# Kernel optimization log

Measured on AMD Instinct MI355X. Metric: run time of the kernel, lower is better.

Reference implementation:

```python
import jax, jax.numpy as jnp
import numpy as np

B, S, D, H = 2, 2048, 1024, 16
E = D // H  # per-head dim_q = dim_k = 64
LN_EPS = 1e-5


def setup_inputs() -> dict:
    key = jax.random.key(0)
    ks = jax.random.split(key, 12)
    s_in = 1.0 / np.sqrt(D)
    s_cat = 1.0 / np.sqrt(H * E)
    return {
        "q": jax.random.normal(ks[0], (B, S, D), jnp.float32),
        "k": jax.random.normal(ks[1], (B, S, D), jnp.float32),
        "v": jax.random.normal(ks[2], (B, S, D), jnp.float32),
        # stacked per-head projection weights [H, D, E] (acts as x @ W + b per head)
        "Wq": jax.random.uniform(ks[3], (H, D, E), jnp.float32, -s_in, s_in),
        "bq": jax.random.uniform(ks[4], (H, E), jnp.float32, -s_in, s_in),
        "Wk": jax.random.uniform(ks[5], (H, D, E), jnp.float32, -s_in, s_in),
        "bk": jax.random.uniform(ks[6], (H, E), jnp.float32, -s_in, s_in),
        "Wv": jax.random.uniform(ks[7], (H, D, E), jnp.float32, -s_in, s_in),
        "bv": jax.random.uniform(ks[8], (H, E), jnp.float32, -s_in, s_in),
        # output linear: [H*E, D]
        "Wo": jax.random.uniform(ks[9], (H * E, D), jnp.float32, -s_cat, s_cat),
        "bo": jax.random.uniform(ks[10], (D,), jnp.float32, -s_cat, s_cat),
        # LayerNorm affine params
        "gamma": jnp.ones((D,), jnp.float32),
        "beta": jnp.zeros((D,), jnp.float32),
    }


def _attention(q, k, v, Wq, bq, Wk, bk, Wv, bv, Wo, bo, gamma, beta):
    # per-head projections: [B,H,S,E]
    qh = jnp.einsum('bsd,hde->bhse', q, Wq) + bq[None, :, None, :]
    kh = jnp.einsum('bsd,hde->bhse', k, Wk) + bk[None, :, None, :]
    vh = jnp.einsum('bsd,hde->bhse', v, Wv) + bv[None, :, None, :]
    scale = jnp.asarray(E, qh.dtype) ** 0.5
    scores = jnp.einsum('bhse,bhte->bhst', qh, kh) / scale  # [B,H,S,S]
    attn = jax.nn.softmax(scores, axis=-1)
    ctx = jnp.einsum('bhst,bhte->bhse', attn, vh)  # [B,H,S,E]
    # concat heads -> [B,S,H*E], then output linear
    cat = ctx.transpose(0, 2, 1, 3).reshape(q.shape[0], q.shape[1], H * E)
    out = cat @ Wo + bo  # [B,S,D]
    # Residual (dropout = identity in eval) + LayerNorm
    x = q + out
    mu = jnp.mean(x, axis=-1, keepdims=True)
    var = jnp.mean((x - mu) ** 2, axis=-1, keepdims=True)
    return (x - mu) * jax.lax.rsqrt(var + LN_EPS) * gamma + beta


def reference(q, k, v, Wq, bq, Wk, bk, Wv, bv, Wo, bo, gamma, beta):
    return _attention(q, k, v, Wq, bq, Wk, bk, Wv, bv, Wo, bo, gamma, beta)
```

## Files before the change

kernel.cpp:

```cpp
#include <hip/hip_runtime.h>
#include <stdint.h>

#define B_  2
#define S_  2048
#define D_  1024
#define H_  16
#define E_  64
#define BH_ 32
#define M_  4096
#define NSPLIT 2
#define KCHUNK (S_ / NSPLIT)

typedef __bf16 bf16x8 __attribute__((ext_vector_type(8)));
typedef float  f32x4  __attribute__((ext_vector_type(4)));
typedef float  f32x16 __attribute__((ext_vector_type(16)));
typedef unsigned short u16;

#define QSCALE 0.180336880f

#define EXP2(x) __builtin_amdgcn_exp2f(x)

__device__ __forceinline__ u16 f2bf(float f) {
  uint32_t u = __builtin_bit_cast(uint32_t, f);
  u = (u + 0x7FFFu + ((u >> 16) & 1u)) >> 16;
  return (u16)u;
}

__device__ __forceinline__ uint32_t pkbf(float lo, float hi) {
  __bf16 a = (__bf16)lo, b = (__bf16)hi;
  return (uint32_t)__builtin_bit_cast(u16, a) |
         ((uint32_t)__builtin_bit_cast(u16, b) << 16);
}

__device__ __forceinline__ bf16x8 load_frag(const u16* p) {
  uint4 v = *(const uint4*)p;
  return __builtin_bit_cast(bf16x8, v);
}

__device__ __forceinline__ float bf2f(u16 u) {
  return __builtin_bit_cast(float, (uint32_t)u << 16);
}

__device__ __forceinline__ void gload16(const void* g, void* l) {
  auto gp = reinterpret_cast<const uint32_t __attribute__((address_space(1)))*>(
      reinterpret_cast<uintptr_t>(g));
  auto lp = reinterpret_cast<uint32_t __attribute__((address_space(3)))*>(
      reinterpret_cast<uintptr_t>(l));
  __builtin_amdgcn_global_load_lds(gp, lp, 16, 0, 0);
}

__global__ __launch_bounds__(256) void transpose_cvt3w(
    const float* __restrict__ Wq, const float* __restrict__ Wk,
    const float* __restrict__ Wv, u16* __restrict__ out)
{
  __shared__ float tile[32][33];
  const int z = blockIdx.z, sel = z >> 4, b = z & 15;
  const float* in = (sel == 0 ? Wq : (sel == 1 ? Wk : Wv)) + (size_t)b * 65536;
  u16* o = out + (size_t)sel * 1048576 + (size_t)b * 65536;
  const int R = 1024, C = 64;
  const int c0 = blockIdx.x * 32, r0 = blockIdx.y * 32;
  const int tx = threadIdx.x, ty = threadIdx.y;
#pragma unroll
  for (int j = 0; j < 32; j += 8)
    tile[ty + j][tx] = in[(size_t)(r0 + ty + j) * C + c0 + tx];
  __syncthreads();
#pragma unroll
  for (int j = 0; j < 32; j += 8)
    o[(size_t)(c0 + ty + j) * R + r0 + tx] = f2bf(tile[tx][ty + j]);
}

__global__ __launch_bounds__(256) void transpose_cvt(
    const float* __restrict__ in, u16* __restrict__ out, int R, int C)
{
  __shared__ float tile[32][33];
  const int c0 = blockIdx.x * 32, r0 = blockIdx.y * 32;
  const int tx = threadIdx.x, ty = threadIdx.y;
#pragma unroll
  for (int j = 0; j < 32; j += 8)
    tile[ty + j][tx] = in[(size_t)(r0 + ty + j) * C + c0 + tx];
  __syncthreads();
#pragma unroll
  for (int j = 0; j < 32; j += 8)
    out[(size_t)(c0 + ty + j) * R + r0 + tx] = f2bf(tile[tx][ty + j]);
}

__global__ __launch_bounds__(256) void cvt3_bf16(
    const float* __restrict__ a, const float* __restrict__ b,
    const float* __restrict__ c, u16* __restrict__ out, int n)
{
  const float* src = blockIdx.y == 0 ? a : (blockIdx.y == 1 ? b : c);
  u16* dst = out + (size_t)blockIdx.y * n;
  int i = (blockIdx.x * 256 + threadIdx.x) * 4;
  if (i < n) {
    float4 v = *(const float4*)(src + i);
    ushort4 o;
    o.x = f2bf(v.x); o.y = f2bf(v.y); o.z = f2bf(v.z); o.w = f2bf(v.w);
    *(ushort4*)(dst + i) = o;
  }
}

template<int MODE>
__global__ __launch_bounds__(256) void gemm128(
    const u16* __restrict__ A, const u16* __restrict__ Bt,
    const float* __restrict__ b0, const float* __restrict__ b1,
    const float* __restrict__ b2, const float* __restrict__ resid,
    u16* __restrict__ outQ, u16* __restrict__ outK, u16* __restrict__ outV,
    float* __restrict__ outX)
{
  __shared__ __align__(16) u16 As[2][128 * 64];
  __shared__ __align__(16) u16 Bs[2][128 * 64];
  const int K  = D_;
  const int id = blockIdx.x;
  const int xcd = id & 7, slot = id >> 3;
  int mi_, ni_;
  if (MODE == 0) { ni_ = slot % 24; mi_ = (xcd << 2) | (slot / 24); }
  else           { ni_ = slot & 7;  mi_ = (xcd << 2) | (slot >> 3); }
  const int m0 = mi_ * 128;
  const int n0 = ni_ * 128;
  const int tid = threadIdx.x;
  const int w = tid >> 6, l = tid & 63;
  const int wr = w >> 1, wc = w & 1;
  const int ql = l & 31, h2 = l >> 5;

  const u16* Ause = A;
  const u16* Buse = Bt;
  const float* bias = b0;
  int third = 0, nloc = n0;
  if (MODE == 0) {
    third = n0 >> 10;
    nloc  = n0 & 1023;
    Ause  = A  + (size_t)third * M_ * D_;
    Buse  = Bt + (size_t)third * D_ * D_;
    bias  = third == 0 ? b0 : (third == 1 ? b1 : b2);
  }

  const int rr = l >> 3, gce = ((l & 7) ^ (l >> 3)) * 8;
  const u16* aptr[4];
  const u16* bptr[4];
#pragma unroll
  for (int c = 0; c < 4; ++c) {
    const int chunk = w * 4 + c;
    aptr[c] = Ause + (size_t)(m0 + chunk * 8 + rr) * K + gce;
    bptr[c] = Buse + (size_t)(nloc + chunk * 8 + rr) * K + gce;
  }

  const int swz = ql & 7;
  f32x16 acc[2][2] = {};

#pragma unroll
  for (int c = 0; c < 4; ++c) {
    const int chunk = w * 4 + c;
    gload16(aptr[c], &As[0][chunk * 8 * 64]);
    gload16(bptr[c], &Bs[0][chunk * 8 * 64]);
  }

  int cur = 0;
  for (int k0 = 0; k0 < K; k0 += 64) {
    __syncthreads();
    const int nxt = k0 + 64;
    if (nxt < K) {
#pragma unroll
      for (int c = 0; c < 4; ++c) {
        const int chunk = w * 4 + c;
        gload16(aptr[c] + nxt, &As[cur ^ 1][chunk * 8 * 64]);
        gload16(bptr[c] + nxt, &Bs[cur ^ 1][chunk * 8 * 64]);
      }
    }
#pragma unroll
    for (int ks = 0; ks < 4; ++ks) {
      const int ch = ((ks * 2 + h2) ^ swz) * 8;
      bf16x8 af[2], bf[2];
#pragma unroll
      for (int mi = 0; mi < 2; ++mi)
        af[mi] = load_frag(&As[cur][(wr * 64 + mi * 32 + ql) * 64 + ch]);
#pragma unroll
      for (int ni = 0; ni < 2; ++ni)
        bf[ni] = load_frag(&Bs[cur][(wc * 64 + ni * 32 + ql) * 64 + ch]);
#pragma unroll
      for (int mi = 0; mi < 2; ++mi)
#pragma unroll
        for (int ni = 0; ni < 2; ++ni)
          acc[mi][ni] = __builtin_amdgcn_mfma_f32_32x32x16_bf16(
              af[mi], bf[ni], acc[mi][ni], 0, 0, 0);
    }
    cur ^= 1;
  }

  const int rbase = m0 + wr * 64;
  const int cbase = nloc + wc * 64;
#pragma unroll
  for (int mi = 0; mi < 2; ++mi) {
#pragma unroll
    for (int ni = 0; ni < 2; ++ni) {
      const int col = cbase + ni * 32 + ql;
      const float bv = bias[col];
      if (MODE == 0) {
        const int h = col >> 6, e = col & 63;
        if (third < 2) {
          u16* dst = third == 0 ? outQ : outK;
          const float sc = third == 0 ? QSCALE : 1.f;
#pragma unroll
          for (int r = 0; r < 16; ++r) {
            int row = rbase + mi * 32 + (r & 3) + 8 * (r >> 2) + 4 * h2;
            int bb = row >> 11, s = row & (S_ - 1);
            dst[((size_t)(bb * H_ + h) * S_ + s) * E_ + e] =
                f2bf((acc[mi][ni][r] + bv) * sc);
          }
        } else {
#pragma unroll
          for (int g = 0; g < 4; ++g) {
            int s0 = rbase + mi * 32 + ((g >> 1) << 4) + (h2 << 3) + ((g & 1) << 2);
            int bb = s0 >> 11, srel = s0 & (S_ - 1);
            ushort4 o;
            o.x = f2bf(acc[mi][ni][4 * g + 0] + bv);
            o.y = f2bf(acc[mi][ni][4 * g + 1] + bv);
            o.z = f2bf(acc[mi][ni][4 * g + 2] + bv);
            o.w = f2bf(acc[mi][ni][4 * g + 3] + bv);
            *(ushort4*)(&outV[((size_t)(bb * H_ + h) * E_ + e) * S_ + srel]) = o;
          }
        }
      } else {
#pragma unroll
        for (int r = 0; r < 16; ++r) {
          int row = rbase + mi * 32 + (r & 3) + 8 * (r >> 2) + 4 * h2;
          size_t idx = (size_t)row * D_ + col;
          outX[idx] = acc[mi][ni][r] + bv + resid[idx];
        }
      }
    }
  }
}

__global__ __launch_bounds__(256, 4) void attn_kernel(
    const u16* __restrict__ qh, const u16* __restrict__ kh,
    const u16* __restrict__ vT, u16* __restrict__ pA,
    float* __restrict__ ml)
{
  __shared__ __align__(16) u16 Ks[2][64 * 64];
  __shared__ __align__(16) u16 Vs[2][64 * 64];
  const int o = blockIdx.x;
  const int xcd = o & 7, slot = o >> 3;
  const int bh    = (xcd << 2) | (slot >> 5);
  const int rem   = slot & 31;
  const int split = rem >> 4;
  const int q0    = (rem & 15) * 128;
  const int kst = split * KCHUNK;
  const int tid = threadIdx.x;
  const int w = tid >> 6, l = tid & 63;
  const int ql = l & 31;
  const int h  = l >> 5;
  const int qg = q0 + w * 32 + ql;

  const size_t PSZ = (size_t)BH_ * S_ * E_;
  u16* po = pA + (size_t)split * PSZ;

  const u16* qrow = qh + ((size_t)bh * S_ + qg) * E_;
  bf16x8 bq_[4];
#pragma unroll
  for (int es = 0; es < 4; ++es)
    bq_[es] = load_frag(qrow + es * 16 + h * 8);

  f32x16 oacc[2] = {};
  float lloc = 0.f;

  const int srow = w * 8 + (l >> 3);
  const int gch  = (l & 7) ^ (l >> 3);
  const u16* kbase = kh + (size_t)bh * S_ * E_;
  const u16* vbase = vT + (size_t)bh * E_ * S_;
  const int swz = (ql & 7);

  auto stage = [&](int buf, int t0) {
#pragma unroll
    for (int p = 0; p < 2; ++p) {
      gload16(kbase + (size_t)(t0 + p * 32 + srow) * E_ + gch * 8,
              &Ks[buf][p * 2048 + w * 512]);
      gload16(vbase + (size_t)(p * 32 + srow) * S_ + t0 + gch * 8,
              &Vs[buf][p * 2048 + w * 512]);
    }
  };

  stage(0, kst);
  int cur = 0;
  for (int t0 = kst; t0 < kst + KCHUNK; t0 += 64) {
    __syncthreads();
    if (t0 + 64 < kst + KCHUNK) stage(cur ^ 1, t0 + 64);

#pragma unroll
    for (int kt = 0; kt < 2; ++kt) {
      f32x16 sacc = {};
#pragma unroll
      for (int es = 0; es < 4; ++es) {
        bf16x8 ak = load_frag(
            &Ks[cur][(kt * 32 + ql) * 64 + (((es * 2 + h) ^ swz) * 8)]);
        sacc = __builtin_amdgcn_mfma_f32_32x32x16_bf16(ak, bq_[es], sacc, 0, 0, 0);
      }

      float ps0 = 0.f, ps1 = 0.f, ps2 = 0.f, ps3 = 0.f;
#pragma unroll
      for (int i = 0; i < 16; i += 4) {
        float p0 = EXP2(sacc[i + 0]); sacc[i + 0] = p0; ps0 += p0;
        float p1 = EXP2(sacc[i + 1]); sacc[i + 1] = p1; ps1 += p1;
        float p2 = EXP2(sacc[i + 2]); sacc[i + 2] = p2; ps2 += p2;
        float p3 = EXP2(sacc[i + 3]); sacc[i + 3] = p3; ps3 += p3;
      }
      lloc += (ps0 + ps1) + (ps2 + ps3);

#pragma unroll
      for (int c2 = 0; c2 < 2; ++c2) {
        uint4 pw;
        pw.x = pkbf(sacc[8 * c2 + 0], sacc[8 * c2 + 1]);
        pw.y = pkbf(sacc[8 * c2 + 2], sacc[8 * c2 + 3]);
        pw.z = pkbf(sacc[8 * c2 + 4], sacc[8 * c2 + 5]);
        pw.w = pkbf(sacc[8 * c2 + 6], sacc[8 * c2 + 7]);
        bf16x8 pb = __builtin_bit_cast(bf16x8, pw);
        const int vch = ((kt * 2 + c2) * 2 + h) ^ swz;
#pragma unroll
        for (int eb = 0; eb < 2; ++eb) {
          bf16x8 av = load_frag(&Vs[cur][(eb * 32 + ql) * 64 + vch * 8]);
          oacc[eb] = __builtin_amdgcn_mfma_f32_32x32x16_bf16(av, pb, oacc[eb], 0, 0, 0);
        }
      }
    }
    cur ^= 1;
  }

  float l_ = lloc + __shfl_xor(lloc, 32);
  const float inv = 1.f / l_;
  const size_t rowbase = ((size_t)bh * S_ + qg) * E_;
#pragma unroll
  for (int eb = 0; eb < 2; ++eb)
#pragma unroll
    for (int g = 0; g < 4; ++g) {
      ushort4 o2;
      o2.x = f2bf(oacc[eb][4 * g + 0] * inv);
      o2.y = f2bf(oacc[eb][4 * g + 1] * inv);
      o2.z = f2bf(oacc[eb][4 * g + 2] * inv);
      o2.w = f2bf(oacc[eb][4 * g + 3] * inv);
      *(ushort4*)(&po[rowbase + eb * 32 + g * 8 + h * 4]) = o2;
    }
  if (h == 0)
    ml[(size_t)(split * BH_ + bh) * S_ + qg] = l_;
}

__global__ __launch_bounds__(256) void combine_kernel(
    const u16* __restrict__ pA, const float* __restrict__ ml,
    u16* __restrict__ cat)
{
  const int idx = blockIdx.x * 256 + threadIdx.x;
  const int e  = (idx & 15) * 4;
  const int s  = (idx >> 4) & (S_ - 1);
  const int bh = idx >> 15;
  const size_t row = (size_t)bh * S_ + s;
  const size_t PSZ = (size_t)BH_ * S_ * E_;

  float li[NSPLIT], W = 0.f;
#pragma unroll
  for (int i = 0; i < NSPLIT; ++i) {
    li[i] = ml[(size_t)(i * BH_ + bh) * S_ + s];
    W += li[i];
  }
  const float invW = 1.f / W;

  float acc0 = 0.f, acc1 = 0.f, acc2 = 0.f, acc3 = 0.f;
#pragma unroll
  for (int i = 0; i < NSPLIT; ++i) {
    const u16* p = pA + (size_t)i * PSZ;
    ushort4 u = *(const ushort4*)(&p[row * E_ + e]);
    const float wi = li[i] * invW;
    acc0 += wi * bf2f(u.x);
    acc1 += wi * bf2f(u.y);
    acc2 += wi * bf2f(u.z);
    acc3 += wi * bf2f(u.w);
  }
  ushort4 o;
  o.x = f2bf(acc0); o.y = f2bf(acc1); o.z = f2bf(acc2); o.w = f2bf(acc3);
  *(ushort4*)(&cat[((size_t)(bh >> 4) * S_ + s) * D_ + (bh & 15) * E_ + e]) = o;
}

__global__ __launch_bounds__(256) void layernorm_kernel(
    float* __restrict__ x, const float* __restrict__ gamma,
    const float* __restrict__ beta)
{
  __shared__ float red[8];
  const int row = blockIdx.x;
  float* p = x + (size_t)row * D_;
  const int tid = threadIdx.x;
  float4 v = *(const float4*)(p + tid * 4);
  float s  = v.x + v.y + v.z + v.w;
  float sq = v.x * v.x + v.y * v.y + v.z * v.z + v.w * v.w;
#pragma unroll
  for (int d = 1; d < 64; d <<= 1) {
    s  += __shfl_xor(s, d);
    sq += __shfl_xor(sq, d);
  }
  const int w = tid >> 6, l = tid & 63;
  if (l == 0) { red[w] = s; red[4 + w] = sq; }
  __syncthreads();
  float S1 = red[0] + red[1] + red[2] + red[3];
  float S2 = red[4] + red[5] + red[6] + red[7];
  float mu  = S1 * (1.f / D_);
  float var = S2 * (1.f / D_) - mu * mu;
  float rinv = rsqrtf(var + 1e-5f);
  float4 g  = *(const float4*)(gamma + tid * 4);
  float4 bt = *(const float4*)(beta + tid * 4);
  float4 o;
  o.x = (v.x - mu) * rinv * g.x + bt.x;
  o.y = (v.y - mu) * rinv * g.y + bt.y;
  o.z = (v.z - mu) * rinv * g.z + bt.z;
  o.w = (v.w - mu) * rinv * g.w + bt.w;
  *(float4*)(p + tid * 4) = o;
}

extern "C" void kernel_launch(void* const* d_in, const int* in_sizes, int n_in,
                              void* d_out, int out_size, void* d_ws, size_t ws_size,
                              hipStream_t stream) {
  (void)in_sizes; (void)n_in; (void)out_size; (void)ws_size;
  const float* q     = (const float*)d_in[0];
  const float* k     = (const float*)d_in[1];
  const float* v     = (const float*)d_in[2];
  const float* Wq    = (const float*)d_in[3];
  const float* bq    = (const float*)d_in[4];
  const float* Wk    = (const float*)d_in[5];
  const float* bk    = (const float*)d_in[6];
  const float* Wv    = (const float*)d_in[7];
  const float* bv    = (const float*)d_in[8];
  const float* Wo    = (const float*)d_in[9];
  const float* bo    = (const float*)d_in[10];
  const float* gamma = (const float*)d_in[11];
  const float* beta  = (const float*)d_in[12];

  char* ws = (char*)d_ws;
  u16* qkv_bf = (u16*)ws;
  u16* Wt     = (u16*)(ws + 25165824);
  u16* WoT    = (u16*)(ws + 31457280);
  u16* qhb    = (u16*)(ws + 33554432);
  u16* khb    = (u16*)(ws + 41943040);
  u16* vTb    = (u16*)(ws + 50331648);
  u16* cat    = qkv_bf;
  u16*   pA  = (u16*)d_out;
  float* mlb = (float*)(ws + 25165824);
  float* x   = (float*)d_out;

  dim3 tb(32, 8);
  transpose_cvt3w<<<dim3(2, 32, 48), tb, 0, stream>>>(Wq, Wk, Wv, Wt);
  transpose_cvt<<<dim3(32, 32, 1), tb, 0, stream>>>(Wo, WoT, 1024, 1024);
  cvt3_bf16<<<dim3(4096, 3), 256, 0, stream>>>(q, k, v, qkv_bf, M_ * D_);

  gemm128<0><<<768, 256, 0, stream>>>(qkv_bf, Wt, bq, bk, bv, nullptr,
                                      qhb, khb, vTb, nullptr);
  attn_kernel<<<1024, 256, 0, stream>>>(qhb, khb, vTb, pA, mlb);
  combine_kernel<<<4096, 256, 0, stream>>>(pA, mlb, cat);
  gemm128<1><<<256, 256, 0, stream>>>(cat, WoT, bo, nullptr, nullptr, q,
                                      nullptr, nullptr, nullptr, x);
  layernorm_kernel<<<4096, 256, 0, stream>>>(x, gamma, beta);
}
```

Before: 147.8 us.

## Drop split-K attention and write context directly into concat layout

Removes the two-way key split in the attention kernel, so each block handles the full key sequence and writes its normalized output straight into the concatenated [B,S,D] buffer. This eliminates the combine kernel, its launch, and the round-trip of partial outputs and row sums through memory. In exchange the grid shrinks from 1024 to 512 blocks, each with twice the loop length, which lowers parallelism and latency hiding across the GPU's compute units.

Measured after the change: 142.6 us. -3.5%, faster.

```diff
diff --git a/kernel.cpp b/kernel.cpp
--- a/kernel.cpp
+++ b/kernel.cpp
@@ -8,8 +8,6 @@
 #define E_  64
 #define BH_ 32
 #define M_  4096
-#define NSPLIT 2
-#define KCHUNK (S_ / NSPLIT)
 
 typedef __bf16 bf16x8 __attribute__((ext_vector_type(8)));
 typedef float  f32x4  __attribute__((ext_vector_type(4)));
@@ -233,27 +231,20 @@
 
 __global__ __launch_bounds__(256, 4) void attn_kernel(
     const u16* __restrict__ qh, const u16* __restrict__ kh,
-    const u16* __restrict__ vT, u16* __restrict__ pA,
-    float* __restrict__ ml)
+    const u16* __restrict__ vT, u16* __restrict__ cat)
 {
   __shared__ __align__(16) u16 Ks[2][64 * 64];
   __shared__ __align__(16) u16 Vs[2][64 * 64];
   const int o = blockIdx.x;
   const int xcd = o & 7, slot = o >> 3;
-  const int bh    = (xcd << 2) | (slot >> 5);
-  const int rem   = slot & 31;
-  const int split = rem >> 4;
-  const int q0    = (rem & 15) * 128;
-  const int kst = split * KCHUNK;
+  const int bh    = (xcd << 2) | (slot >> 4);
+  const int q0    = (slot & 15) * 128;
   const int tid = threadIdx.x;
   const int w = tid >> 6, l = tid & 63;
   const int ql = l & 31;
   const int h  = l >> 5;
   const int qg = q0 + w * 32 + ql;
 
-  const size_t PSZ = (size_t)BH_ * S_ * E_;
-  u16* po = pA + (size_t)split * PSZ;
-
   const u16* qrow = qh + ((size_t)bh * S_ + qg) * E_;
   bf16x8 bq_[4];
 #pragma unroll
@@ -279,11 +270,11 @@
     }
   };
 
-  stage(0, kst);
+  stage(0, 0);
   int cur = 0;
-  for (int t0 = kst; t0 < kst + KCHUNK; t0 += 64) {
+  for (int t0 = 0; t0 < S_; t0 += 64) {
     __syncthreads();
-    if (t0 + 64 < kst + KCHUNK) stage(cur ^ 1, t0 + 64);
+    if (t0 + 64 < S_) stage(cur ^ 1, t0 + 64);
 
 #pragma unroll
     for (int kt = 0; kt < 2; ++kt) {
@@ -326,7 +317,8 @@
 
   float l_ = lloc + __shfl_xor(lloc, 32);
   const float inv = 1.f / l_;
-  const size_t rowbase = ((size_t)bh * S_ + qg) * E_;
+  const int bb = bh >> 4, hh = bh & 15;
+  const size_t rowbase = ((size_t)bb * S_ + qg) * D_ + hh * E_;
 #pragma unroll
   for (int eb = 0; eb < 2; ++eb)
 #pragma unroll
@@ -336,45 +328,8 @@
       o2.y = f2bf(oacc[eb][4 * g + 1] * inv);
       o2.z = f2bf(oacc[eb][4 * g + 2] * inv);
       o2.w = f2bf(oacc[eb][4 * g + 3] * inv);
-      *(ushort4*)(&po[rowbase + eb * 32 + g * 8 + h * 4]) = o2;
-    }
-  if (h == 0)
-    ml[(size_t)(split * BH_ + bh) * S_ + qg] = l_;
-}
-
-__global__ __launch_bounds__(256) void combine_kernel(
-    const u16* __restrict__ pA, const float* __restrict__ ml,
-    u16* __restrict__ cat)
-{
-  const int idx = blockIdx.x * 256 + threadIdx.x;
-  const int e  = (idx & 15) * 4;
-  const int s  = (idx >> 4) & (S_ - 1);
-  const int bh = idx >> 15;
-  const size_t row = (size_t)bh * S_ + s;
-  const size_t PSZ = (size_t)BH_ * S_ * E_;
-
-  float li[NSPLIT], W = 0.f;
-#pragma unroll
-  for (int i = 0; i < NSPLIT; ++i) {
-    li[i] = ml[(size_t)(i * BH_ + bh) * S_ + s];
-    W += li[i];
-  }
-  const float invW = 1.f / W;
-
-  float acc0 = 0.f, acc1 = 0.f, acc2 = 0.f, acc3 = 0.f;
-#pragma unroll
-  for (int i = 0; i < NSPLIT; ++i) {
-    const u16* p = pA + (size_t)i * PSZ;
-    ushort4 u = *(const ushort4*)(&p[row * E_ + e]);
-    const float wi = li[i] * invW;
-    acc0 += wi * bf2f(u.x);
-    acc1 += wi * bf2f(u.y);
-    acc2 += wi * bf2f(u.z);
-    acc3 += wi * bf2f(u.w);
-  }
-  ushort4 o;
-  o.x = f2bf(acc0); o.y = f2bf(acc1); o.z = f2bf(acc2); o.w = f2bf(acc3);
-  *(ushort4*)(&cat[((size_t)(bh >> 4) * S_ + s) * D_ + (bh & 15) * E_ + e]) = o;
+      *(ushort4*)(&cat[rowbase + eb * 32 + g * 8 + h * 4]) = o2;
+    }
 }
 
 __global__ __launch_bounds__(256) void layernorm_kernel(
@@ -437,9 +392,7 @@
   u16* khb    = (u16*)(ws + 41943040);
   u16* vTb    = (u16*)(ws + 50331648);
   u16* cat    = qkv_bf;
-  u16*   pA  = (u16*)d_out;
-  float* mlb = (float*)(ws + 25165824);
-  float* x   = (float*)d_out;
+  float* x    = (float*)d_out;
 
   dim3 tb(32, 8);
   transpose_cvt3w<<<dim3(2, 32, 48), tb, 0, stream>>>(Wq, Wk, Wv, Wt);
@@ -448,8 +401,7 @@
 
   gemm128<0><<<768, 256, 0, stream>>>(qkv_bf, Wt, bq, bk, bv, nullptr,
                                       qhb, khb, vTb, nullptr);
-  attn_kernel<<<1024, 256, 0, stream>>>(qhb, khb, vTb, pA, mlb);
-  combine_kernel<<<4096, 256, 0, stream>>>(pA, mlb, cat);
+  attn_kernel<<<512, 256, 0, stream>>>(qhb, khb, vTb, cat);
   gemm128<1><<<256, 256, 0, stream>>>(cat, WoT, bo, nullptr, nullptr, q,
                                       nullptr, nullptr, nullptr, x);
   layernorm_kernel<<<4096, 256, 0, stream>>>(x, gamma, beta);
```
